# Optimization experiments

Hardware: AMD Instinct MI355X
Metric: run time of the kernel (lower is better)

Reference implementation:

```python
import jax, jax.numpy as jnp
import numpy as np

SIDE_LEN = 128
RESOLUTION = 1.0  # Angstrom per pixel


def setup_inputs() -> dict:
    key = jax.random.key(0)
    k1, k2, k3 = jax.random.split(key, 3)
    B, A = 16, 20000
    # atom xyz coords in Angstrom, spread within the field of view (+/- 63.5 A)
    mol = jax.random.normal(k1, (B, A, 3), dtype=jnp.float32) * 20.0
    # per-atom Gaussian std in [0.5, 1.5) A (strictly positive)
    stds = jax.random.uniform(k2, (A,), dtype=jnp.float32) + 0.5
    # per-atom density (mass) in [0.5, 1.5)
    densities = jax.random.uniform(k3, (A,), dtype=jnp.float32) + 0.5
    return {"mol": mol, "stds": stds, "densities": densities}


def reference(mol, stds, densities):
    # Pixel-center coordinate grid, identical to torch.arange(-x_max, x_max+1e-5, res)
    x_max = (SIDE_LEN - 1) * RESOLUTION / 2
    coord = jnp.arange(-x_max, x_max + 1e-5, RESOLUTION, dtype=jnp.float32)  # (S,)
    var = stds * stds                              # (A,)
    neg_half_inv_var = (-0.5 / var)[None, :, None] # (1,A,1)
    # Separable Gaussian profiles: exp(-(coord - mu)^2 / (2 var))
    dx = coord[None, None, :] - mol[:, :, 0:1]     # (B,A,S) x-offsets
    dy = coord[None, None, :] - mol[:, :, 1:2]     # (B,A,S) y-offsets
    gx = jnp.exp(neg_half_inv_var * dx * dx)       # (B,A,W)
    gy = jnp.exp(neg_half_inv_var * dy * dy)       # (B,A,H)
    coef = densities / (2.0 * jnp.pi * var)        # (A,)
    # img[b,h,w] = sum_a coef_a * gy[b,a,h] * gx[b,a,w]  (batched matmul)
    img = jnp.einsum('bah,baw->bhw', gy * coef[None, :, None], gx)
    return img  # (B, SIDE_LEN, SIDE_LEN)
```

## Files before the change

### kernel.cpp

```cpp
#include <hip/hip_runtime.h>


#define S 128
#define NS 32
#define PER 640
#define BLOCK 512
#define KC 32
#define GSTR 40

typedef _Float16 f16;
typedef _Float16 f16x2 __attribute__((ext_vector_type(2)));
typedef _Float16 f16x8 __attribute__((ext_vector_type(8)));
typedef float floatx16 __attribute__((ext_vector_type(16)));

#if __has_builtin(__builtin_amdgcn_exp2f)
#define FAST_EXP2(x) __builtin_amdgcn_exp2f(x)
#else
#define FAST_EXP2(x) exp2f(x)
#endif
#if __has_builtin(__builtin_amdgcn_rcpf)
#define FAST_RCP(x) __builtin_amdgcn_rcpf(x)
#else
#define FAST_RCP(x) (1.0f / (x))
#endif

static __device__ __forceinline__ f16x2 PKRTZ(float a, float b) {
#if __has_builtin(__builtin_amdgcn_cvt_pkrtz)
    return __builtin_bit_cast(f16x2, __builtin_amdgcn_cvt_pkrtz(a, b));
#else
    return (f16x2){(f16)a, (f16)b};
#endif
}

union frag_u { f16x8 v; f16x2 h[4]; };

union SharedU {
    struct {
        float4 sG[2][PER];
        f16 g[2][2][S * GSTR];
    } m;
    float red[4 * 4096];
};

__global__ __launch_bounds__(BLOCK, 4) void k_proj(
    const float* __restrict__ mol,
    const float* __restrict__ stds,
    const float* __restrict__ dens,
    f16* __restrict__ part,
    int B, int A)
{
    __shared__ SharedU sh;

    const int ks   = blockIdx.x;
    const int b    = blockIdx.y;
    const int tid  = threadIdx.x;
    const int lane = tid & 63;
    const int wav  = tid >> 6;
    const int quad = wav & 3;
    const int half = wav >> 2;
    const int l31  = lane & 31;
    const int hi   = lane >> 5;

    const int a0  = ks * PER;
    const int a1  = min(a0 + PER, A);
    const int cnt = a1 - a0;

    for (int i = tid; i < cnt; i += BLOCK) {
        const int a = a0 + i;
        const size_t idx = (size_t)b * A + a;
        float x  = mol[idx * 3 + 0];
        float y  = mol[idx * 3 + 1];
        float v  = stds[a] * stds[a];
        float rv = FAST_RCP(v);
        float z  = -0.72134752044448f * rv;
        float w  = __log2f(dens[a] * 0.15915494309189535f * rv);
        sh.m.sG[0][i] = make_float4(x, z, 0.f, 0.f);
        sh.m.sG[1][i] = make_float4(y, z, w,   0.f);
    }
    __syncthreads();

    const int nc = cnt >> 5;

    const int gaxis = wav >> 2;
    const int agrp  = wav & 3;
    const float c0  = (float)lane - 63.5f;

    const int arow = (quad >> 1) * 64 + l31;
    const int acol = (quad & 1) * 64 + l31;
    const int aoff = half * 16 + hi * 8;

    floatx16 acc[2][2];
#pragma unroll
    for (int rr = 0; rr < 2; ++rr)
#pragma unroll
        for (int cb = 0; cb < 2; ++cb) acc[rr][cb] = (floatx16){0.f};

    auto GEN_COMPUTE = [&](int c, frag_u& V0, frag_u& V1) {
        const float4* prm = &sh.m.sG[gaxis][c * KC + agrp * 8];
#pragma unroll
        for (int i2 = 0; i2 < 4; ++i2) {
            float e0[2], e1[2];
#pragma unroll
            for (int u = 0; u < 2; ++u) {
                float4 p = prm[i2 * 2 + u];
                float d  = c0 - p.x;
                float t  = p.y * d;
                float g0 = fmaf(t, d, p.z);
                float g1 = fmaf(128.0f, t, fmaf(4096.0f, p.y, g0));
                e0[u] = FAST_EXP2(g0);
                e1[u] = FAST_EXP2(g1);
            }
            V0.h[i2] = PKRTZ(e0[0], e0[1]);
            V1.h[i2] = PKRTZ(e1[0], e1[1]);
        }
    };

#define STEP(P)                                                                \
    do {                                                                       \
        const f16* gy = sh.m.g[(P)][1];                                        \
        const f16* gx = sh.m.g[(P)][0];                                        \
        const bool gen = (c + 1 < nc);                                         \
        frag_u V0, V1;                                                         \
        if (gen) GEN_COMPUTE(c + 1, V0, V1);                                   \
        frag_u A0, A1, B0, B1;                                                 \
        A0.v = *(const f16x8*)(gy + arow * GSTR + aoff);                       \
        A1.v = *(const f16x8*)(gy + (arow + 32) * GSTR + aoff);                \
        B0.v = *(const f16x8*)(gx + acol * GSTR + aoff);                       \
        B1.v = *(const f16x8*)(gx + (acol + 32) * GSTR + aoff);                \
        acc[0][0] = __builtin_amdgcn_mfma_f32_32x32x16_f16(A0.v, B0.v, acc[0][0], 0, 0, 0); \
        acc[0][1] = __builtin_amdgcn_mfma_f32_32x32x16_f16(A0.v, B1.v, acc[0][1], 0, 0, 0); \
        acc[1][0] = __builtin_amdgcn_mfma_f32_32x32x16_f16(A1.v, B0.v, acc[1][0], 0, 0, 0); \
        acc[1][1] = __builtin_amdgcn_mfma_f32_32x32x16_f16(A1.v, B1.v, acc[1][1], 0, 0, 0); \
        if (gen) {                                                             \
            f16* dst = &sh.m.g[(P) ^ 1][gaxis][lane * GSTR + agrp * 8];        \
            *(f16x8*)dst               = V0.v;                                 \
            *(f16x8*)(dst + 64 * GSTR) = V1.v;                                 \
        }                                                                      \
        __syncthreads();                                                       \
        ++c;                                                                   \
    } while (0)

    {
        frag_u V0, V1;
        GEN_COMPUTE(0, V0, V1);
        f16* dst = &sh.m.g[0][gaxis][lane * GSTR + agrp * 8];
        *(f16x8*)dst               = V0.v;
        *(f16x8*)(dst + 64 * GSTR) = V1.v;
    }
    __syncthreads();

    int c = 0;
    while (c + 2 <= nc) { STEP(0); STEP(1); }
    if (c < nc) STEP(0);
#undef STEP

    float* rq = sh.red + quad * 4096;
    if (half == 0) {
#pragma unroll
        for (int rr = 0; rr < 2; ++rr)
#pragma unroll
            for (int cb = 0; cb < 2; ++cb) {
                float* t = rq + (rr * 2 + cb) * 1024 + lane;
#pragma unroll
                for (int j = 0; j < 16; ++j) t[j * 64] = acc[rr][cb][j];
            }
    }
    __syncthreads();

    if (half == 1) {
        f16* base = part + ((size_t)(b * NS + ks)) * (S * S) + lane * 16;
#pragma unroll
        for (int rr = 0; rr < 2; ++rr)
#pragma unroll
            for (int cb = 0; cb < 2; ++cb) {
                float* t = rq + (rr * 2 + cb) * 1024 + lane;
                floatx16 v = acc[rr][cb];
#pragma unroll
                for (int j = 0; j < 16; ++j) v[j] += t[j * 64];
                const int tileidx = ((quad >> 1) * 2 + rr) * 4 + ((quad & 1) * 2 + cb);
                f16* pq = base + (size_t)tileidx * 1024;
                frag_u lo, hiv;
#pragma unroll
                for (int jp = 0; jp < 4; ++jp) {
                    lo.h[jp]  = PKRTZ(v[2 * jp],     v[2 * jp + 1]);
                    hiv.h[jp] = PKRTZ(v[2 * jp + 8], v[2 * jp + 9]);
                }
                *(f16x8*)(pq + 0) = lo.v;
                *(f16x8*)(pq + 8) = hiv.v;
            }
    }
}

__global__ __launch_bounds__(256) void k_reduce(const f16* __restrict__ part,
                                                float* __restrict__ out) {
    __shared__ float lred[3][64][9];
    const int b    = blockIdx.z;
    const int lane = threadIdx.x & 63;
    const int w    = threadIdx.x >> 6;
    const int f8   = (blockIdx.x * 64 + lane) * 8;

    const f16* src = part + (size_t)b * NS * (S * S) + (size_t)(w * 8) * (S * S) + f8;
    float s[8] = {0.f};
#pragma unroll
    for (int t = 0; t < 8; ++t) {
        f16x8 v = *(const f16x8*)&src[(size_t)t * (S * S)];
#pragma unroll
        for (int i = 0; i < 8; ++i) s[i] += (float)v[i];
    }

    if (w) {
#pragma unroll
        for (int i = 0; i < 8; ++i) lred[w - 1][lane][i] = s[i];
    }
    __syncthreads();

    if (w == 0) {
#pragma unroll
        for (int j = 0; j < 3; ++j)
#pragma unroll
            for (int i = 0; i < 8; ++i) s[i] += lred[j][lane][i];

        const int reg0   = f8 & 15;
        const int lane_f = (f8 >> 4) & 63;
        const int tile   = f8 >> 10;
        const int r      = tile >> 2;
        const int cc     = tile & 3;
        const int rowb = r * 32 + 4 * (lane_f >> 5);
        const int col  = cc * 32 + (lane_f & 31);
#pragma unroll
        for (int i = 0; i < 8; ++i) {
            const int reg = reg0 + i;
            const int row = rowb + (reg & 3) + 8 * (reg >> 2);
            out[((size_t)b * S + row) * S + col] = s[i];
        }
    }
}

extern "C" void kernel_launch(void* const* d_in, const int* in_sizes, int n_in,
                              void* d_out, int out_size, void* d_ws, size_t ws_size,
                              hipStream_t stream) {
    const float* mol  = (const float*)d_in[0];
    const float* stds = (const float*)d_in[1];
    const float* dens = (const float*)d_in[2];
    float* out = (float*)d_out;

    const int A = in_sizes[1];
    const int B = in_sizes[0] / (A * 3);

    f16* part = (f16*)d_ws;

    k_proj<<<dim3(NS, B), dim3(BLOCK), 0, stream>>>(mol, stds, dens, part, B, A);
    k_reduce<<<dim3((S * S) / (64 * 8), 1, B), dim3(256), 0, stream>>>(part, out);
}
```

Before: 88.53 us.

## Fuse projection and reduction into one cooperative kernel with grid sync

Merges the projection kernel and the split-K reduction kernel into a single cooperative launch. A grid-wide sync separates the two phases, and each of the 512 blocks then reduces one slice of the partial images, with 8 waves each summing 4 partials. The goal is to remove the second kernel launch and its gap. In exchange it adds grid-sync cost and depends on all 512 blocks being co-resident; if the cooperative launch fails, it falls back to the two-kernel path.

```diff
diff --git a/kernel.cpp b/kernel.cpp
--- a/kernel.cpp
+++ b/kernel.cpp
@@ -1,4 +1,5 @@
 #include <hip/hip_runtime.h>
+#include <hip/hip_cooperative_groups.h>
 
 
 #define S 128
@@ -7,6 +8,8 @@
 #define BLOCK 512
 #define KC 32
 #define GSTR 40
+
+namespace cg = cooperative_groups;
 
 typedef _Float16 f16;
 typedef _Float16 f16x2 __attribute__((ext_vector_type(2)));
@@ -40,17 +43,14 @@
         f16 g[2][2][S * GSTR];
     } m;
     float red[4 * 4096];
+    float lred[7][64][9];
 };
 
-__global__ __launch_bounds__(BLOCK, 4) void k_proj(
-    const float* __restrict__ mol,
-    const float* __restrict__ stds,
-    const float* __restrict__ dens,
-    f16* __restrict__ part,
-    int B, int A)
+template <typename SH>
+static __device__ __forceinline__ void proj_body(
+    SH& sh, const float* __restrict__ mol, const float* __restrict__ stds,
+    const float* __restrict__ dens, f16* __restrict__ part, int B, int A)
 {
-    __shared__ SharedU sh;
-
     const int ks   = blockIdx.x;
     const int b    = blockIdx.y;
     const int tid  = threadIdx.x;
@@ -191,6 +191,69 @@
     }
 }
 
+__global__ __launch_bounds__(BLOCK, 4) void k_fused(
+    const float* __restrict__ mol, const float* __restrict__ stds,
+    const float* __restrict__ dens, f16* __restrict__ part,
+    float* __restrict__ out, int B, int A)
+{
+    __shared__ SharedU sh;
+    proj_body(sh, mol, stds, dens, part, B, A);
+
+    cg::this_grid().sync();
+
+    const int tid  = threadIdx.x;
+    const int lane = tid & 63;
+    const int wav  = tid >> 6;
+    const int rb   = blockIdx.y * NS + blockIdx.x;
+    const int rbx  = rb & 31;
+    const int rbb  = rb >> 5;
+    const int f8   = (rbx * 64 + lane) * 8;
+
+    const f16* src = part + (size_t)rbb * NS * (S * S) + (size_t)(wav * 4) * (S * S) + f8;
+    float s[8] = {0.f};
+#pragma unroll
+    for (int t = 0; t < 4; ++t) {
+        f16x8 v = *(const f16x8*)&src[(size_t)t * (S * S)];
+#pragma unroll
+        for (int i = 0; i < 8; ++i) s[i] += (float)v[i];
+    }
+
+    if (wav) {
+#pragma unroll
+        for (int i = 0; i < 8; ++i) sh.lred[wav - 1][lane][i] = s[i];
+    }
+    __syncthreads();
+
+    if (wav == 0) {
+#pragma unroll
+        for (int j = 0; j < 7; ++j)
+#pragma unroll
+            for (int i = 0; i < 8; ++i) s[i] += sh.lred[j][lane][i];
+
+        const int reg0   = f8 & 15;
+        const int lane_f = (f8 >> 4) & 63;
+        const int tile   = f8 >> 10;
+        const int r      = tile >> 2;
+        const int cc     = tile & 3;
+        const int rowb = r * 32 + 4 * (lane_f >> 5);
+        const int col  = cc * 32 + (lane_f & 31);
+#pragma unroll
+        for (int i = 0; i < 8; ++i) {
+            const int reg = reg0 + i;
+            const int row = rowb + (reg & 3) + 8 * (reg >> 2);
+            out[((size_t)rbb * S + row) * S + col] = s[i];
+        }
+    }
+}
+
+__global__ __launch_bounds__(BLOCK, 4) void k_proj(
+    const float* __restrict__ mol, const float* __restrict__ stds,
+    const float* __restrict__ dens, f16* __restrict__ part, int B, int A)
+{
+    __shared__ SharedU sh;
+    proj_body(sh, mol, stds, dens, part, B, A);
+}
+
 __global__ __launch_bounds__(256) void k_reduce(const f16* __restrict__ part,
                                                 float* __restrict__ out) {
     __shared__ float lred[3][64][9];
@@ -244,11 +307,19 @@
     const float* dens = (const float*)d_in[2];
     float* out = (float*)d_out;
 
-    const int A = in_sizes[1];
-    const int B = in_sizes[0] / (A * 3);
+    int A = in_sizes[1];
+    int B = in_sizes[0] / (A * 3);
 
     f16* part = (f16*)d_ws;
 
-    k_proj<<<dim3(NS, B), dim3(BLOCK), 0, stream>>>(mol, stds, dens, part, B, A);
-    k_reduce<<<dim3((S * S) / (64 * 8), 1, B), dim3(256), 0, stream>>>(part, out);
-}
+    void* args[] = {(void*)&mol, (void*)&stds, (void*)&dens,
+                    (void*)&part, (void*)&out, (void*)&B, (void*)&A};
+    hipError_t e = hipLaunchCooperativeKernel((const void*)k_fused,
+                                              dim3(NS, B), dim3(BLOCK),
+                                              args, 0, stream);
+    if (e != hipSuccess) {
+        (void)hipGetLastError();
+        k_proj<<<dim3(NS, B), dim3(BLOCK), 0, stream>>>(mol, stds, dens, part, B, A);
+        k_reduce<<<dim3((S * S) / (64 * 8), 1, B), dim3(256), 0, stream>>>(part, out);
+    }
+}
```

After: 154.4 us. +74.4%, slower.

## Process two atom chunks per barrier and pack per-atom params into one float4

Applied to the files above, without the earlier changes.

The shared Gaussian tile now holds two 32-atom chunks per buffer (stride widened to 68), so each barrier covers two chunks of generation plus MFMA instead of one, halving __syncthreads count. Per-atom parameters are merged into a single float4 array selected by axis, which shrinks the parameter table in LDS. Shared loads and stores are split into 8-byte halves to fit the new stride alignment, which raises LDS instruction count and LDS footprint per block and may affect occupancy.

```diff
diff --git a/kernel.cpp b/kernel.cpp
--- a/kernel.cpp
+++ b/kernel.cpp
@@ -6,10 +6,11 @@
 #define PER 640
 #define BLOCK 512
 #define KC 32
-#define GSTR 40
+#define GSTR 68
 
 typedef _Float16 f16;
 typedef _Float16 f16x2 __attribute__((ext_vector_type(2)));
+typedef _Float16 f16x4 __attribute__((ext_vector_type(4)));
 typedef _Float16 f16x8 __attribute__((ext_vector_type(8)));
 typedef float floatx16 __attribute__((ext_vector_type(16)));
 
@@ -32,11 +33,11 @@
 #endif
 }
 
-union frag_u { f16x8 v; f16x2 h[4]; };
+union frag_u { f16x8 v; f16x4 q[2]; f16x2 h[4]; };
 
 union SharedU {
     struct {
-        float4 sG[2][PER];
+        float4 sG[PER];
         f16 g[2][2][S * GSTR];
     } m;
     float red[4 * 4096];
@@ -74,8 +75,7 @@
         float rv = FAST_RCP(v);
         float z  = -0.72134752044448f * rv;
         float w  = __log2f(dens[a] * 0.15915494309189535f * rv);
-        sh.m.sG[0][i] = make_float4(x, z, 0.f, 0.f);
-        sh.m.sG[1][i] = make_float4(y, z, w,   0.f);
+        sh.m.sG[i] = make_float4(x, y, z, w);
     }
     __syncthreads();
 
@@ -95,64 +95,79 @@
 #pragma unroll
         for (int cb = 0; cb < 2; ++cb) acc[rr][cb] = (floatx16){0.f};
 
-    auto GEN_COMPUTE = [&](int c, frag_u& V0, frag_u& V1) {
-        const float4* prm = &sh.m.sG[gaxis][c * KC + agrp * 8];
+    auto GEN_CHUNK = [&](int c, int par) {
+        const float4* prm = &sh.m.sG[c * KC + agrp * 8];
+        frag_u V0, V1;
 #pragma unroll
         for (int i2 = 0; i2 < 4; ++i2) {
             float e0[2], e1[2];
 #pragma unroll
             for (int u = 0; u < 2; ++u) {
                 float4 p = prm[i2 * 2 + u];
-                float d  = c0 - p.x;
-                float t  = p.y * d;
-                float g0 = fmaf(t, d, p.z);
-                float g1 = fmaf(128.0f, t, fmaf(4096.0f, p.y, g0));
+                float mu = gaxis ? p.y : p.x;
+                float wc = gaxis ? p.w : 0.0f;
+                float d  = c0 - mu;
+                float t  = p.z * d;
+                float g0 = fmaf(t, d, wc);
+                float g1 = fmaf(128.0f, t, fmaf(4096.0f, p.z, g0));
                 e0[u] = FAST_EXP2(g0);
                 e1[u] = FAST_EXP2(g1);
             }
             V0.h[i2] = PKRTZ(e0[0], e0[1]);
             V1.h[i2] = PKRTZ(e1[0], e1[1]);
         }
+        f16* dst = &sh.m.g[par][gaxis][lane * GSTR + (c & 1) * 32 + agrp * 8];
+        *(f16x4*)(dst)     = V0.q[0];
+        *(f16x4*)(dst + 4) = V0.q[1];
+        f16* dst2 = dst + 64 * GSTR;
+        *(f16x4*)(dst2)     = V1.q[0];
+        *(f16x4*)(dst2 + 4) = V1.q[1];
     };
 
-#define STEP(P)                                                                \
+#define CHUNK_MFMA(gy, gx, qq)                                                 \
     do {                                                                       \
-        const f16* gy = sh.m.g[(P)][1];                                        \
-        const f16* gx = sh.m.g[(P)][0];                                        \
-        const bool gen = (c + 1 < nc);                                         \
-        frag_u V0, V1;                                                         \
-        if (gen) GEN_COMPUTE(c + 1, V0, V1);                                   \
         frag_u A0, A1, B0, B1;                                                 \
-        A0.v = *(const f16x8*)(gy + arow * GSTR + aoff);                       \
-        A1.v = *(const f16x8*)(gy + (arow + 32) * GSTR + aoff);                \
-        B0.v = *(const f16x8*)(gx + acol * GSTR + aoff);                       \
-        B1.v = *(const f16x8*)(gx + (acol + 32) * GSTR + aoff);                \
+        const f16* ay = (gy) + arow * GSTR + (qq) * 32 + aoff;                 \
+        const f16* ax = (gx) + acol * GSTR + (qq) * 32 + aoff;                 \
+        A0.q[0] = *(const f16x4*)(ay);                                         \
+        A0.q[1] = *(const f16x4*)(ay + 4);                                     \
+        A1.q[0] = *(const f16x4*)(ay + 32 * GSTR);                             \
+        A1.q[1] = *(const f16x4*)(ay + 32 * GSTR + 4);                         \
+        B0.q[0] = *(const f16x4*)(ax);                                         \
+        B0.q[1] = *(const f16x4*)(ax + 4);                                     \
+        B1.q[0] = *(const f16x4*)(ax + 32 * GSTR);                             \
+        B1.q[1] = *(const f16x4*)(ax + 32 * GSTR + 4);                         \
         acc[0][0] = __builtin_amdgcn_mfma_f32_32x32x16_f16(A0.v, B0.v, acc[0][0], 0, 0, 0); \
         acc[0][1] = __builtin_amdgcn_mfma_f32_32x32x16_f16(A0.v, B1.v, acc[0][1], 0, 0, 0); \
         acc[1][0] = __builtin_amdgcn_mfma_f32_32x32x16_f16(A1.v, B0.v, acc[1][0], 0, 0, 0); \
         acc[1][1] = __builtin_amdgcn_mfma_f32_32x32x16_f16(A1.v, B1.v, acc[1][1], 0, 0, 0); \
-        if (gen) {                                                             \
-            f16* dst = &sh.m.g[(P) ^ 1][gaxis][lane * GSTR + agrp * 8];        \
-            *(f16x8*)dst               = V0.v;                                 \
-            *(f16x8*)(dst + 64 * GSTR) = V1.v;                                 \
-        }                                                                      \
+    } while (0)
+
+#define STEP2(PAR)                                                             \
+    do {                                                                       \
+        const f16* gy = sh.m.g[(PAR)][1];                                      \
+        const f16* gx = sh.m.g[(PAR)][0];                                      \
+        if (c + 2 < nc) GEN_CHUNK(c + 2, (PAR) ^ 1);                           \
+        CHUNK_MFMA(gy, gx, 0);                                                 \
+        if (c + 3 < nc) GEN_CHUNK(c + 3, (PAR) ^ 1);                           \
+        if (c + 1 < nc) CHUNK_MFMA(gy, gx, 1);                                 \
         __syncthreads();                                                       \
-        ++c;                                                                   \
+        c += 2;                                                                \
     } while (0)
 
-    {
-        frag_u V0, V1;
-        GEN_COMPUTE(0, V0, V1);
-        f16* dst = &sh.m.g[0][gaxis][lane * GSTR + agrp * 8];
-        *(f16x8*)dst               = V0.v;
-        *(f16x8*)(dst + 64 * GSTR) = V1.v;
-    }
+    GEN_CHUNK(0, 0);
+    if (nc > 1) GEN_CHUNK(1, 0);
     __syncthreads();
 
     int c = 0;
-    while (c + 2 <= nc) { STEP(0); STEP(1); }
-    if (c < nc) STEP(0);
-#undef STEP
+    for (;;) {
+        STEP2(0);
+        if (c >= nc) break;
+        STEP2(1);
+        if (c >= nc) break;
+    }
+#undef STEP2
+#undef CHUNK_MFMA
 
     float* rq = sh.red + quad * 4096;
     if (half == 0) {
@@ -231,7 +246,7 @@
         for (int i = 0; i < 8; ++i) {
             const int reg = reg0 + i;
             const int row = rowb + (reg & 3) + 8 * (reg >> 2);
-            out[((size_t)b * S + row) * S + col] = s[i];
+            out[((size_t)b * S + row) * S + col] = s[i] ;
         }
     }
 }
```

Result: no change. 88.65 us (+0.1%).

## Use 1024-thread blocks with one 32x32 output tile per wave

Applied to the files above, without the earlier changes.

Doubles the block to 16 waves, each owning a single 32x32 output tile over the full K chunk instead of 2x2 tiles split across two K halves. This removes the shared-memory cross-wave accumulator reduction and its extra barrier, and packs the per-atom parameters into one float4 array. The cost is that each wave now generates only 4 atoms per step, and the 1024-thread block with per-step barriers may cut occupancy or add synchronisation overhead. Fewer MFMA instructions per wave per step also reduce latency hiding.

```diff
diff --git a/kernel.cpp b/kernel.cpp
--- a/kernel.cpp
+++ b/kernel.cpp
@@ -4,12 +4,13 @@
 #define S 128
 #define NS 32
 #define PER 640
-#define BLOCK 512
+#define BLOCK 1024
 #define KC 32
 #define GSTR 40
 
 typedef _Float16 f16;
 typedef _Float16 f16x2 __attribute__((ext_vector_type(2)));
+typedef _Float16 f16x4 __attribute__((ext_vector_type(4)));
 typedef _Float16 f16x8 __attribute__((ext_vector_type(8)));
 typedef float floatx16 __attribute__((ext_vector_type(16)));
 
@@ -32,32 +33,28 @@
 #endif
 }
 
-union frag_u { f16x8 v; f16x2 h[4]; };
-
-union SharedU {
-    struct {
-        float4 sG[2][PER];
-        f16 g[2][2][S * GSTR];
-    } m;
-    float red[4 * 4096];
+union frag_u { f16x8 v; f16x4 q[2]; f16x2 h[4]; };
+union half4_u { f16x4 q; f16x2 h[2]; };
+
+struct SharedT {
+    float4 sG[PER];
+    f16 g[2][2][S * GSTR];
 };
 
-__global__ __launch_bounds__(BLOCK, 4) void k_proj(
+__global__ __launch_bounds__(BLOCK, 8) void k_proj(
     const float* __restrict__ mol,
     const float* __restrict__ stds,
     const float* __restrict__ dens,
     f16* __restrict__ part,
     int B, int A)
 {
-    __shared__ SharedU sh;
+    __shared__ SharedT sh;
 
     const int ks   = blockIdx.x;
     const int b    = blockIdx.y;
     const int tid  = threadIdx.x;
     const int lane = tid & 63;
     const int wav  = tid >> 6;
-    const int quad = wav & 3;
-    const int half = wav >> 2;
     const int l31  = lane & 31;
     const int hi   = lane >> 5;
 
@@ -74,39 +71,36 @@
         float rv = FAST_RCP(v);
         float z  = -0.72134752044448f * rv;
         float w  = __log2f(dens[a] * 0.15915494309189535f * rv);
-        sh.m.sG[0][i] = make_float4(x, z, 0.f, 0.f);
-        sh.m.sG[1][i] = make_float4(y, z, w,   0.f);
+        sh.sG[i] = make_float4(x, y, z, w);
     }
     __syncthreads();
 
     const int nc = cnt >> 5;
 
-    const int gaxis = wav >> 2;
-    const int agrp  = wav & 3;
+    const int gaxis = wav >> 3;
+    const int agrp  = wav & 7;
     const float c0  = (float)lane - 63.5f;
 
-    const int arow = (quad >> 1) * 64 + l31;
-    const int acol = (quad & 1) * 64 + l31;
-    const int aoff = half * 16 + hi * 8;
-
-    floatx16 acc[2][2];
-#pragma unroll
-    for (int rr = 0; rr < 2; ++rr)
-#pragma unroll
-        for (int cb = 0; cb < 2; ++cb) acc[rr][cb] = (floatx16){0.f};
-
-    auto GEN_COMPUTE = [&](int c, frag_u& V0, frag_u& V1) {
-        const float4* prm = &sh.m.sG[gaxis][c * KC + agrp * 8];
-#pragma unroll
-        for (int i2 = 0; i2 < 4; ++i2) {
+    const int arow = (wav >> 2) * 32 + l31;
+    const int bcol = (wav & 3) * 32 + l31;
+    const int koff = hi * 8;
+
+    floatx16 acc = (floatx16){0.f};
+
+    auto GEN_COMPUTE = [&](int c, half4_u& V0, half4_u& V1) {
+        const float4* prm = &sh.sG[c * KC + agrp * 4];
+#pragma unroll
+        for (int i2 = 0; i2 < 2; ++i2) {
             float e0[2], e1[2];
 #pragma unroll
             for (int u = 0; u < 2; ++u) {
                 float4 p = prm[i2 * 2 + u];
-                float d  = c0 - p.x;
-                float t  = p.y * d;
-                float g0 = fmaf(t, d, p.z);
-                float g1 = fmaf(128.0f, t, fmaf(4096.0f, p.y, g0));
+                float mu = gaxis ? p.y : p.x;
+                float wc = gaxis ? p.w : 0.0f;
+                float d  = c0 - mu;
+                float t  = p.z * d;
+                float g0 = fmaf(t, d, wc);
+                float g1 = fmaf(128.0f, t, fmaf(4096.0f, p.z, g0));
                 e0[u] = FAST_EXP2(g0);
                 e1[u] = FAST_EXP2(g1);
             }
@@ -117,35 +111,33 @@
 
 #define STEP(P)                                                                \
     do {                                                                       \
-        const f16* gy = sh.m.g[(P)][1];                                        \
-        const f16* gx = sh.m.g[(P)][0];                                        \
+        const f16* gy = sh.g[(P)][1];                                          \
+        const f16* gx = sh.g[(P)][0];                                          \
         const bool gen = (c + 1 < nc);                                         \
-        frag_u V0, V1;                                                         \
+        half4_u V0, V1;                                                        \
         if (gen) GEN_COMPUTE(c + 1, V0, V1);                                   \
-        frag_u A0, A1, B0, B1;                                                 \
-        A0.v = *(const f16x8*)(gy + arow * GSTR + aoff);                       \
-        A1.v = *(const f16x8*)(gy + (arow + 32) * GSTR + aoff);                \
-        B0.v = *(const f16x8*)(gx + acol * GSTR + aoff);                       \
-        B1.v = *(const f16x8*)(gx + (acol + 32) * GSTR + aoff);                \
-        acc[0][0] = __builtin_amdgcn_mfma_f32_32x32x16_f16(A0.v, B0.v, acc[0][0], 0, 0, 0); \
-        acc[0][1] = __builtin_amdgcn_mfma_f32_32x32x16_f16(A0.v, B1.v, acc[0][1], 0, 0, 0); \
-        acc[1][0] = __builtin_amdgcn_mfma_f32_32x32x16_f16(A1.v, B0.v, acc[1][0], 0, 0, 0); \
-        acc[1][1] = __builtin_amdgcn_mfma_f32_32x32x16_f16(A1.v, B1.v, acc[1][1], 0, 0, 0); \
+        _Pragma("unroll")                                                      \
+        for (int s = 0; s < 2; ++s) {                                          \
+            frag_u Af, Bf;                                                     \
+            Af.v = *(const f16x8*)(gy + arow * GSTR + s * 16 + koff);          \
+            Bf.v = *(const f16x8*)(gx + bcol * GSTR + s * 16 + koff);          \
+            acc = __builtin_amdgcn_mfma_f32_32x32x16_f16(Af.v, Bf.v, acc, 0, 0, 0); \
+        }                                                                      \
         if (gen) {                                                             \
-            f16* dst = &sh.m.g[(P) ^ 1][gaxis][lane * GSTR + agrp * 8];        \
-            *(f16x8*)dst               = V0.v;                                 \
-            *(f16x8*)(dst + 64 * GSTR) = V1.v;                                 \
+            f16* dst = &sh.g[(P) ^ 1][gaxis][lane * GSTR + agrp * 4];          \
+            *(f16x4*)dst               = V0.q;                                 \
+            *(f16x4*)(dst + 64 * GSTR) = V1.q;                                 \
         }                                                                      \
         __syncthreads();                                                       \
         ++c;                                                                   \
     } while (0)
 
     {
-        frag_u V0, V1;
+        half4_u V0, V1;
         GEN_COMPUTE(0, V0, V1);
-        f16* dst = &sh.m.g[0][gaxis][lane * GSTR + agrp * 8];
-        *(f16x8*)dst               = V0.v;
-        *(f16x8*)(dst + 64 * GSTR) = V1.v;
+        f16* dst = &sh.g[0][gaxis][lane * GSTR + agrp * 4];
+        *(f16x4*)dst               = V0.q;
+        *(f16x4*)(dst + 64 * GSTR) = V1.q;
     }
     __syncthreads();
 
@@ -154,40 +146,17 @@
     if (c < nc) STEP(0);
 #undef STEP
 
-    float* rq = sh.red + quad * 4096;
-    if (half == 0) {
-#pragma unroll
-        for (int rr = 0; rr < 2; ++rr)
-#pragma unroll
-            for (int cb = 0; cb < 2; ++cb) {
-                float* t = rq + (rr * 2 + cb) * 1024 + lane;
-#pragma unroll
-                for (int j = 0; j < 16; ++j) t[j * 64] = acc[rr][cb][j];
-            }
-    }
-    __syncthreads();
-
-    if (half == 1) {
-        f16* base = part + ((size_t)(b * NS + ks)) * (S * S) + lane * 16;
-#pragma unroll
-        for (int rr = 0; rr < 2; ++rr)
-#pragma unroll
-            for (int cb = 0; cb < 2; ++cb) {
-                float* t = rq + (rr * 2 + cb) * 1024 + lane;
-                floatx16 v = acc[rr][cb];
-#pragma unroll
-                for (int j = 0; j < 16; ++j) v[j] += t[j * 64];
-                const int tileidx = ((quad >> 1) * 2 + rr) * 4 + ((quad & 1) * 2 + cb);
-                f16* pq = base + (size_t)tileidx * 1024;
-                frag_u lo, hiv;
-#pragma unroll
-                for (int jp = 0; jp < 4; ++jp) {
-                    lo.h[jp]  = PKRTZ(v[2 * jp],     v[2 * jp + 1]);
-                    hiv.h[jp] = PKRTZ(v[2 * jp + 8], v[2 * jp + 9]);
-                }
-                *(f16x8*)(pq + 0) = lo.v;
-                *(f16x8*)(pq + 8) = hiv.v;
-            }
+    {
+        f16* pq = part + ((size_t)(b * NS + ks)) * (S * S)
+                       + (size_t)wav * 1024 + lane * 16;
+        frag_u lo, hiv;
+#pragma unroll
+        for (int jp = 0; jp < 4; ++jp) {
+            lo.h[jp]  = PKRTZ(acc[2 * jp],     acc[2 * jp + 1]);
+            hiv.h[jp] = PKRTZ(acc[2 * jp + 8], acc[2 * jp + 9]);
+        }
+        *(f16x8*)(pq + 0) = lo.v;
+        *(f16x8*)(pq + 8) = hiv.v;
     }
 }
 
```

Result: faster. 85.65 us, median of 2 (-3.3%).
